# Kernel tuning notes

Measured on AMD Instinct MI355X. Metric: run time of the kernel, lower is better.

## Reference

```python
import jax, jax.numpy as jnp
import numpy as np

B, S, E, H, SN, LMAX = 128, 512, 768, 16, 100, 5
DH = E // H  # 48

def setup_inputs() -> dict:
    key = jax.random.key(0)
    ks = jax.random.split(key, 10)
    idx = jax.random.randint(ks[0], (B, LMAX), 0, S)
    lengths = jax.random.randint(ks[1], (B,), 1, LMAX + 1)
    valid = jnp.arange(LMAX)[None, :] < lengths[:, None]
    locations = jnp.where(valid, idx, -1)
    return {
        "last_hidden_state": jax.random.normal(ks[2], (B, S, E), jnp.float32),
        "sense_emb": jax.random.normal(ks[3], (B, SN, E), jnp.float32),
        "locations": locations,
        "in_proj_weight": jax.random.normal(ks[4], (3 * E, E), jnp.float32) * 0.02,
        "in_proj_bias": jax.random.normal(ks[5], (3 * E,), jnp.float32) * 0.02,
        "out_proj_weight": jax.random.normal(ks[6], (E, E), jnp.float32) * 0.02,
        "out_proj_bias": jax.random.normal(ks[7], (E,), jnp.float32) * 0.02,
        "linear_weight": jax.random.normal(ks[8], (SN, E), jnp.float32) * 0.02,
        "linear_bias": jax.random.normal(ks[9], (SN,), jnp.float32) * 0.02,
    }

def reference(last_hidden_state, sense_emb, locations, in_proj_weight, in_proj_bias,
              out_proj_weight, out_proj_bias, linear_weight, linear_bias):
    # Ragged gather + mean over the valid (non -1) token locations per row.
    mask = (locations != -1)                                   # [B, LMAX]
    safe = jnp.where(mask, locations, 0)                       # [B, LMAX]
    gathered = jnp.take_along_axis(last_hidden_state, safe[..., None], axis=1)  # [B,LMAX,E]
    cnt = mask.sum(axis=1, keepdims=True).astype(last_hidden_state.dtype)
    pun = (gathered * mask[..., None]).sum(axis=1) / cnt       # [B, E]

    # qkv: prepend pun-word embedding to the sense embeddings -> [B, SN+1, E]
    qkv = jnp.concatenate([pun[:, None, :], sense_emb], axis=1)

    # nn.MultiheadAttention with batch_first=False: axis0 = seq (L=B), axis1 = batch (N=SN+1).
    proj = qkv @ in_proj_weight.T + in_proj_bias               # [L, N, 3E]
    q, k, v = jnp.split(proj, 3, axis=-1)
    L, N = qkv.shape[0], qkv.shape[1]
    q = q.reshape(L, N, H, DH) * (DH ** -0.5)
    k = k.reshape(L, N, H, DH)
    v = v.reshape(L, N, H, DH)
    scores = jnp.einsum('lnhd,mnhd->nhlm', q, k)               # [N,H,L,L]
    attn = jax.nn.softmax(scores, axis=-1)
    ctx = jnp.einsum('nhlm,mnhd->lnhd', attn, v).reshape(L, N, E)
    attn_out = ctx @ out_proj_weight.T + out_proj_bias         # [L, N, E]

    res = attn_out[:, 0, :]                                    # [B, E] (batch slot 0)
    res = res @ linear_weight.T + linear_bias                  # [B, SN]
    return res
```

## Files before the change

kernel.cpp:

```cpp
#include <hip/hip_runtime.h>

#define SEQ 512
#define EMB 768
#define K3E 2304
#define DHD 48

__global__ __launch_bounds__(256) void k0_pun(
    const float* __restrict__ lhs, const int* __restrict__ loc,
    float* __restrict__ pun)
{
  int id = blockIdx.x * 256 + threadIdx.x;
  int row = id / 192;
  int ch  = id - row * 192;
  int cnt = 0;
  float4 s = make_float4(0.f, 0.f, 0.f, 0.f);
#pragma unroll
  for (int j = 0; j < 5; j++) {
    int v = loc[row * 5 + j];
    if (v >= 0) {
      float4 wv = *(const float4*)&lhs[((size_t)row * SEQ + v) * EMB + ch * 4];
      s.x += wv.x; s.y += wv.y; s.z += wv.z; s.w += wv.w;
      cnt++;
    }
  }
  float inv = 1.0f / (float)cnt;
  *(float4*)&pun[(size_t)row * EMB + ch * 4] =
      make_float4(s.x * inv, s.y * inv, s.z * inv, s.w * inv);
}

__global__ __launch_bounds__(512, 4) void k1_gemm_wcomb(
    const float* __restrict__ pun, const float* __restrict__ Bw,
    const float* __restrict__ bias, float* __restrict__ C,
    const float* __restrict__ wlin, const float* __restrict__ wout,
    float* __restrict__ wcomb)
{
  __shared__ float lds[12288];
  const int t = threadIdx.x;
  const int w = t >> 6, l = t & 63;
  const int h2 = l >> 5;
  const int tx = l & 7;
  const int ty = (l >> 3) & 3;
  const int gm = l & 15, gq = l >> 4;
  const int bl = l & 31, bh = l >> 5;
  const int kbase = w * 96;
  const int AW = w * 1536, BW = AW + 512;

  float4 aF, bF0, bF1;
  float acc[4][4] = {};

#define STAGE_A(b) {                                                         \
    int Ab = AW + (b) * 256;                                                 \
    lds[Ab + (gq*4+0)*16 + gm] = aF.x;                                       \
    lds[Ab + (gq*4+1)*16 + gm] = aF.y;                                       \
    lds[Ab + (gq*4+2)*16 + gm] = aF.z;                                       \
    lds[Ab + (gq*4+3)*16 + gm] = aF.w; }

#define INNER(b) {                                                           \
    int Ab = AW + (b) * 256, Bb = BW + (b) * 512;                            \
    _Pragma("unroll")                                                        \
    for (int kk = 0; kk < 8; kk++) {                                         \
      int row = kk * 2 + h2;                                                 \
      float4 a  = *(float4*)&lds[Ab + row * 16 + ty * 4];                    \
      float4 bb = *(float4*)&lds[Bb + row * 32 + tx * 4];                    \
      acc[0][0] += a.x*bb.x; acc[0][1] += a.x*bb.y;                          \
      acc[0][2] += a.x*bb.z; acc[0][3] += a.x*bb.w;                          \
      acc[1][0] += a.y*bb.x; acc[1][1] += a.y*bb.y;                          \
      acc[1][2] += a.y*bb.z; acc[1][3] += a.y*bb.w;                          \
      acc[2][0] += a.z*bb.x; acc[2][1] += a.z*bb.y;                          \
      acc[2][2] += a.z*bb.z; acc[2][3] += a.z*bb.w;                          \
      acc[3][0] += a.w*bb.x; acc[3][1] += a.w*bb.y;                          \
      acc[3][2] += a.w*bb.z; acc[3][3] += a.w*bb.w;                          \
    } }

#define FOLD_AND_PARTIAL() {                                                 \
    _Pragma("unroll")                                                        \
    for (int i = 0; i < 4; i++) {                                            \
      _Pragma("unroll")                                                      \
      for (int j = 0; j < 4; j++)                                            \
        acc[i][j] += __shfl_xor(acc[i][j], 32);                              \
    }                                                                        \
    if (l < 32) {                                                            \
      _Pragma("unroll")                                                      \
      for (int i = 0; i < 4; i++)                                            \
        *(float4*)&lds[AW + (ty*4 + i) * 32 + tx * 4] =                      \
            make_float4(acc[i][0], acc[i][1], acc[i][2], acc[i][3]);         \
    }                                                                        \
    __syncthreads(); }

  if (blockIdx.x < 576) {
    const int c  = blockIdx.x;
    const int bm = (c / 72) * 16, bn = (c % 72) * 32;
    const float* arow = pun + (size_t)(bm + gm) * EMB;
    const float* brow = Bw + (size_t)(bn + bl) * EMB;

#define G_LOAD(s) {                                                          \
    int k0 = kbase + (s) * 16;                                               \
    aF  = *(const float4*)&arow[k0 + gq * 4];                                \
    bF0 = *(const float4*)&brow[k0 + bh * 8 + 0];                            \
    bF1 = *(const float4*)&brow[k0 + bh * 8 + 4]; }

#define G_WRITE(b) {                                                         \
    STAGE_A(b)                                                               \
    int Bb = BW + (b) * 512;                                                 \
    lds[Bb + (bh*8+0)*32 + bl] = bF0.x; lds[Bb + (bh*8+1)*32 + bl] = bF0.y;  \
    lds[Bb + (bh*8+2)*32 + bl] = bF0.z; lds[Bb + (bh*8+3)*32 + bl] = bF0.w;  \
    lds[Bb + (bh*8+4)*32 + bl] = bF1.x; lds[Bb + (bh*8+5)*32 + bl] = bF1.y;  \
    lds[Bb + (bh*8+6)*32 + bl] = bF1.z; lds[Bb + (bh*8+7)*32 + bl] = bF1.w; }

    G_LOAD(0); G_WRITE(0);
    for (int s = 0; s < 6; s++) {
      int b = s & 1;
      if (s < 5) G_LOAD(s + 1);
      INNER(b);
      if (s < 5) G_WRITE(b ^ 1);
    }
#undef G_LOAD
#undef G_WRITE

    FOLD_AND_PARTIAL();
    int m = t >> 5, n = t & 31;
    float v = lds[0*1536 + t] + lds[1*1536 + t] + lds[2*1536 + t] + lds[3*1536 + t]
            + lds[4*1536 + t] + lds[5*1536 + t] + lds[6*1536 + t] + lds[7*1536 + t]
            + bias[bn + n];
    C[(size_t)(bm + m) * K3E + bn + n] = v;
  } else {
    const int cc = blockIdx.x - 576;
    const int bm = (cc / 24) * 16, bn = (cc % 24) * 32;
    const int wi = l >> 2;
    const int j4 = (l & 3) * 8;
    int arow_i = bm + gm; if (arow_i > 99) arow_i = 99;
    const float* arow = wlin + (size_t)arow_i * EMB;

#define W_LOAD(s) {                                                          \
    int k0 = kbase + (s) * 16;                                               \
    aF  = *(const float4*)&arow[k0 + gq * 4];                                \
    const float* wr = wout + (size_t)(k0 + wi) * EMB + bn + j4;              \
    bF0 = *(const float4*)&wr[0];                                            \
    bF1 = *(const float4*)&wr[4]; }

#define W_WRITE(b) {                                                         \
    STAGE_A(b)                                                               \
    int Bb = BW + (b) * 512;                                                 \
    *(float4*)&lds[Bb + wi*32 + j4]     = bF0;                               \
    *(float4*)&lds[Bb + wi*32 + j4 + 4] = bF1; }

    W_LOAD(0); W_WRITE(0);
    for (int s = 0; s < 6; s++) {
      int b = s & 1;
      if (s < 5) W_LOAD(s + 1);
      INNER(b);
      if (s < 5) W_WRITE(b ^ 1);
    }
#undef W_LOAD
#undef W_WRITE

    FOLD_AND_PARTIAL();
    int m = t >> 5, n = t & 31;
    if (bm + m < 100) {
      float v = lds[0*1536 + t] + lds[1*1536 + t] + lds[2*1536 + t] + lds[3*1536 + t]
              + lds[4*1536 + t] + lds[5*1536 + t] + lds[6*1536 + t] + lds[7*1536 + t];
      wcomb[(size_t)(bm + m) * EMB + bn + n] = v;
    }
  }
#undef STAGE_A
#undef INNER
#undef FOLD_AND_PARTIAL
}

__global__ __launch_bounds__(256) void k2_attn(
    const float* __restrict__ proj, float* __restrict__ ctx)
{
  __shared__ float ks[128][52];
  __shared__ float vs[128][52];
  int h  = blockIdx.x >> 3;
  int l0 = (blockIdx.x & 7) * 16;
  int t  = threadIdx.x;

  for (int i = t; i < 128 * 12; i += 256) {
    int m  = i / 12;
    int dd = (i - m * 12) * 4;
    float4 kv = *(const float4*)&proj[(size_t)m * K3E + EMB     + h * DHD + dd];
    float4 vv = *(const float4*)&proj[(size_t)m * K3E + 2 * EMB + h * DHD + dd];
    *(float4*)&ks[m][dd] = kv;
    *(float4*)&vs[m][dd] = vv;
  }

  int l  = t >> 4;
  int g  = t & 15;
  int lg = l0 + l;
  const float scale = 0.14433756729740643f;
  float q[48];
#pragma unroll
  for (int jj = 0; jj < 12; jj++) {
    float4 qv = *(const float4*)&proj[(size_t)lg * K3E + h * DHD + jj * 4];
    q[jj*4+0] = qv.x * scale; q[jj*4+1] = qv.y * scale;
    q[jj*4+2] = qv.z * scale; q[jj*4+3] = qv.w * scale;
  }
  __syncthreads();

  float sv[8];
  float smax = -1e30f;
#pragma unroll
  for (int jm = 0; jm < 8; jm++) {
    int m = g + jm * 16;
    float s = 0.0f;
#pragma unroll
    for (int dq = 0; dq < 12; dq++) {
      float4 kv = *(const float4*)&ks[m][dq * 4];
      s += q[dq*4+0]*kv.x + q[dq*4+1]*kv.y + q[dq*4+2]*kv.z + q[dq*4+3]*kv.w;
    }
    sv[jm] = s;
    smax = fmaxf(smax, s);
  }
#pragma unroll
  for (int off = 1; off < 16; off <<= 1) smax = fmaxf(smax, __shfl_xor(smax, off));
  float ssum = 0.0f;
#pragma unroll
  for (int jm = 0; jm < 8; jm++) { float e = __expf(sv[jm] - smax); sv[jm] = e; ssum += e; }
#pragma unroll
  for (int off = 1; off < 16; off <<= 1) ssum += __shfl_xor(ssum, off);
  float inv = 1.0f / ssum;
#pragma unroll
  for (int jm = 0; jm < 8; jm++) sv[jm] *= inv;

  float acc[48] = {};
#pragma unroll
  for (int jm = 0; jm < 8; jm++) {
    int m = g + jm * 16;
    float p = sv[jm];
#pragma unroll
    for (int dq = 0; dq < 12; dq++) {
      float4 vv = *(const float4*)&vs[m][dq * 4];
      acc[dq*4+0] += p*vv.x; acc[dq*4+1] += p*vv.y;
      acc[dq*4+2] += p*vv.z; acc[dq*4+3] += p*vv.w;
    }
  }

  {
    float buf[24];
    if (g & 8) {
#pragma unroll
      for (int d = 0; d < 24; d++) buf[d] = acc[d];
    } else {
#pragma unroll
      for (int d = 0; d < 24; d++) buf[d] = acc[d + 24];
    }
#pragma unroll
    for (int d = 0; d < 24; d++) buf[d] = __shfl_xor(buf[d], 8);
    if (g & 8) {
#pragma unroll
      for (int d = 0; d < 24; d++) acc[d] = acc[d + 24] + buf[d];
    } else {
#pragma unroll
      for (int d = 0; d < 24; d++) acc[d] = acc[d] + buf[d];
    }
  }
  {
    float buf[12];
    if (g & 4) {
#pragma unroll
      for (int d = 0; d < 12; d++) buf[d] = acc[d];
    } else {
#pragma unroll
      for (int d = 0; d < 12; d++) buf[d] = acc[d + 12];
    }
#pragma unroll
    for (int d = 0; d < 12; d++) buf[d] = __shfl_xor(buf[d], 4);
    if (g & 4) {
#pragma unroll
      for (int d = 0; d < 12; d++) acc[d] = acc[d + 12] + buf[d];
    } else {
#pragma unroll
      for (int d = 0; d < 12; d++) acc[d] = acc[d] + buf[d];
    }
  }
  {
    float buf[6];
    if (g & 2) {
#pragma unroll
      for (int d = 0; d < 6; d++) buf[d] = acc[d];
    } else {
#pragma unroll
      for (int d = 0; d < 6; d++) buf[d] = acc[d + 6];
    }
#pragma unroll
    for (int d = 0; d < 6; d++) buf[d] = __shfl_xor(buf[d], 2);
    if (g & 2) {
#pragma unroll
      for (int d = 0; d < 6; d++) acc[d] = acc[d + 6] + buf[d];
    } else {
#pragma unroll
      for (int d = 0; d < 6; d++) acc[d] = acc[d] + buf[d];
    }
  }
  {
    float buf[3];
    if (g & 1) {
#pragma unroll
      for (int d = 0; d < 3; d++) buf[d] = acc[d];
    } else {
#pragma unroll
      for (int d = 0; d < 3; d++) buf[d] = acc[d + 3];
    }
#pragma unroll
    for (int d = 0; d < 3; d++) buf[d] = __shfl_xor(buf[d], 1);
    if (g & 1) {
#pragma unroll
      for (int d = 0; d < 3; d++) acc[d] = acc[d + 3] + buf[d];
    } else {
#pragma unroll
      for (int d = 0; d < 3; d++) acc[d] = acc[d] + buf[d];
    }
  }
#pragma unroll
  for (int j = 0; j < 3; j++) {
    ctx[(size_t)lg * EMB + h * DHD + g * 3 + j] = acc[j];
  }
}

__global__ __launch_bounds__(512, 4) void k3_final(
    const float* __restrict__ A, const float* __restrict__ Bw,
    const float* __restrict__ wlin, const float* __restrict__ bout,
    const float* __restrict__ blin, float* __restrict__ C)
{
  __shared__ float lds[14368];
  const int t = threadIdx.x;
  const int w = t >> 6, l = t & 63;
  const int bm = blockIdx.y * 16, bn = blockIdx.x * 32;
  const int tx = l & 7, ty = l >> 3;
  const int gm = l & 15, gq = l >> 4;
  const int bl = l & 31, bh = l >> 5;
  const int kbase = w * 96;
  const int AW = w * 1792, BW = AW + 640;

  if (t < 256) {
    int col = bn + (t >> 3);
    int ks  = (t & 7) * 96;
    float p = 0.f;
    if (col < 100) {
      const float* wr = wlin + (size_t)col * EMB + ks;
#pragma unroll
      for (int j = 0; j < 24; j++) {
        float4 wv = *(const float4*)&wr[j * 4];
        float4 bv = *(const float4*)&bout[ks + j * 4];
        p += wv.x*bv.x + wv.y*bv.y + wv.z*bv.z + wv.w*bv.w;
      }
    }
    p += __shfl_xor(p, 1); p += __shfl_xor(p, 2); p += __shfl_xor(p, 4);
    if ((t & 7) == 0) lds[14336 + (t >> 3)] = p + (col < 100 ? blin[col] : 0.f);
  }

  const float* arow = A + (size_t)(bm + gm) * EMB;
  int brow_i = bn + bl; if (brow_i > 99) brow_i = 99;
  const float* brow = Bw + (size_t)brow_i * EMB;

  float4 aF, bF0, bF1;

#define F_LOAD(s) {                                                          \
    int k0 = kbase + (s) * 16;                                               \
    aF  = *(const float4*)&arow[k0 + gq * 4];                                \
    bF0 = *(const float4*)&brow[k0 + bh * 8 + 0];                            \
    bF1 = *(const float4*)&brow[k0 + bh * 8 + 4]; }

#define F_WRITE(b) {                                                         \
    int Ab = AW + (b) * 320;                                                 \
    lds[Ab + (gq*4+0)*20 + gm] = aF.x;                                       \
    lds[Ab + (gq*4+1)*20 + gm] = aF.y;                                       \
    lds[Ab + (gq*4+2)*20 + gm] = aF.z;                                       \
    lds[Ab + (gq*4+3)*20 + gm] = aF.w;                                       \
    int Bb = BW + (b) * 576;                                                 \
    lds[Bb + (bh*8+0)*36 + bl] = bF0.x; lds[Bb + (bh*8+1)*36 + bl] = bF0.y;  \
    lds[Bb + (bh*8+2)*36 + bl] = bF0.z; lds[Bb + (bh*8+3)*36 + bl] = bF0.w;  \
    lds[Bb + (bh*8+4)*36 + bl] = bF1.x; lds[Bb + (bh*8+5)*36 + bl] = bF1.y;  \
    lds[Bb + (bh*8+6)*36 + bl] = bF1.z; lds[Bb + (bh*8+7)*36 + bl] = bF1.w; }

  float acc[2][4] = {};
  F_LOAD(0); F_WRITE(0);
  for (int s = 0; s < 6; s++) {
    int b = s & 1;
    if (s < 5) F_LOAD(s + 1);
    int Ab = AW + b * 320, Bb = BW + b * 576;
#pragma unroll
    for (int kk = 0; kk < 16; kk++) {
      float2 a  = *(float2*)&lds[Ab + kk * 20 + ty * 2];
      float4 bb = *(float4*)&lds[Bb + kk * 36 + tx * 4];
      acc[0][0] += a.x*bb.x; acc[0][1] += a.x*bb.y; acc[0][2] += a.x*bb.z; acc[0][3] += a.x*bb.w;
      acc[1][0] += a.y*bb.x; acc[1][1] += a.y*bb.y; acc[1][2] += a.y*bb.z; acc[1][3] += a.y*bb.w;
    }
    if (s < 5) F_WRITE(b ^ 1);
  }
#undef F_LOAD
#undef F_WRITE

#pragma unroll
  for (int i = 0; i < 2; i++)
    *(float4*)&lds[AW + (ty*2 + i) * 32 + tx * 4] =
        make_float4(acc[i][0], acc[i][1], acc[i][2], acc[i][3]);
  __syncthreads();
  int m = t >> 5, n = t & 31;
  int col = bn + n;
  if (col < 100) {
    float v = lds[0*1792 + t] + lds[1*1792 + t] + lds[2*1792 + t] + lds[3*1792 + t]
            + lds[4*1792 + t] + lds[5*1792 + t] + lds[6*1792 + t] + lds[7*1792 + t]
            + lds[14336 + n];
    C[(size_t)(bm + m) * 100 + col] = v;
  }
}

extern "C" void kernel_launch(void* const* d_in, const int* in_sizes, int n_in,
                              void* d_out, int out_size, void* d_ws, size_t ws_size,
                              hipStream_t stream) {
  const float* lhs   = (const float*)d_in[0];
  const int*   loc   = (const int*)  d_in[2];
  const float* w_in  = (const float*)d_in[3];
  const float* b_in  = (const float*)d_in[4];
  const float* w_out = (const float*)d_in[5];
  const float* b_out = (const float*)d_in[6];
  const float* w_lin = (const float*)d_in[7];
  const float* b_lin = (const float*)d_in[8];
  float* out = (float*)d_out;

  char* ws = (char*)d_ws;
  float* pun   = (float*)(ws);
  float* proj  = (float*)(ws + 393216);
  float* ctx   = (float*)(ws + 1572864);
  float* wcomb = (float*)(ws + 1966080);

  k0_pun<<<96, 256, 0, stream>>>(lhs, loc, pun);
  k1_gemm_wcomb<<<744, 512, 0, stream>>>(pun, w_in, b_in, proj,
                                         w_lin, w_out, wcomb);
  k2_attn<<<128, 256, 0, stream>>>(proj, ctx);
  k3_final<<<dim3(4, 8), 512, 0, stream>>>(ctx, wcomb, w_lin, b_out, b_lin, out);
}
```

Measured before the change: 45.58 us.

## Fuse attention and final GEMM into one kernel with per-row-block flag sync

Merges the attention kernel and the final projection GEMM into a single launch of 160 blocks. The first 128 blocks compute attention and bump a per-row-tile counter after writing ctx. The remaining 32 blocks precompute the bias term, spin on that counter, then run the GEMM with 256 threads instead of 512. This removes one kernel launch boundary and lets the final GEMM for a row tile start as soon as its 16 attention blocks finish. The risks are spin-wait deadlock if the consumer blocks occupy slots before the producers run, and the cost of a half-size thread block in the GEMM. Flags are reset in the first kernel.

```diff
diff --git a/kernel.cpp b/kernel.cpp
--- a/kernel.cpp
+++ b/kernel.cpp
@@ -7,8 +7,11 @@
 
 __global__ __launch_bounds__(256) void k0_pun(
     const float* __restrict__ lhs, const int* __restrict__ loc,
-    float* __restrict__ pun)
+    float* __restrict__ pun, int* __restrict__ flags)
 {
+  if (blockIdx.x == 0 && threadIdx.x < 8)
+    __hip_atomic_store(&flags[threadIdx.x], 0, __ATOMIC_RELAXED,
+                       __HIP_MEMORY_SCOPE_AGENT);
   int id = blockIdx.x * 256 + threadIdx.x;
   int row = id / 192;
   int ch  = id - row * 192;
@@ -167,243 +170,261 @@
 #undef FOLD_AND_PARTIAL
 }
 
-__global__ __launch_bounds__(256) void k2_attn(
-    const float* __restrict__ proj, float* __restrict__ ctx)
+__global__ __launch_bounds__(256) void k23_attn_final(
+    const float* __restrict__ proj, const float* __restrict__ wcomb,
+    const float* __restrict__ wlin, const float* __restrict__ bout,
+    const float* __restrict__ blin, float* __restrict__ ctx,
+    float* __restrict__ out, int* __restrict__ flags)
 {
-  __shared__ float ks[128][52];
-  __shared__ float vs[128][52];
-  int h  = blockIdx.x >> 3;
-  int l0 = (blockIdx.x & 7) * 16;
-  int t  = threadIdx.x;
-
-  for (int i = t; i < 128 * 12; i += 256) {
-    int m  = i / 12;
-    int dd = (i - m * 12) * 4;
-    float4 kv = *(const float4*)&proj[(size_t)m * K3E + EMB     + h * DHD + dd];
-    float4 vv = *(const float4*)&proj[(size_t)m * K3E + 2 * EMB + h * DHD + dd];
-    *(float4*)&ks[m][dd] = kv;
-    *(float4*)&vs[m][dd] = vv;
-  }
-
-  int l  = t >> 4;
-  int g  = t & 15;
-  int lg = l0 + l;
-  const float scale = 0.14433756729740643f;
-  float q[48];
-#pragma unroll
-  for (int jj = 0; jj < 12; jj++) {
-    float4 qv = *(const float4*)&proj[(size_t)lg * K3E + h * DHD + jj * 4];
-    q[jj*4+0] = qv.x * scale; q[jj*4+1] = qv.y * scale;
-    q[jj*4+2] = qv.z * scale; q[jj*4+3] = qv.w * scale;
-  }
-  __syncthreads();
-
-  float sv[8];
-  float smax = -1e30f;
-#pragma unroll
-  for (int jm = 0; jm < 8; jm++) {
-    int m = g + jm * 16;
-    float s = 0.0f;
-#pragma unroll
-    for (int dq = 0; dq < 12; dq++) {
-      float4 kv = *(const float4*)&ks[m][dq * 4];
-      s += q[dq*4+0]*kv.x + q[dq*4+1]*kv.y + q[dq*4+2]*kv.z + q[dq*4+3]*kv.w;
-    }
-    sv[jm] = s;
-    smax = fmaxf(smax, s);
-  }
-#pragma unroll
-  for (int off = 1; off < 16; off <<= 1) smax = fmaxf(smax, __shfl_xor(smax, off));
-  float ssum = 0.0f;
-#pragma unroll
-  for (int jm = 0; jm < 8; jm++) { float e = __expf(sv[jm] - smax); sv[jm] = e; ssum += e; }
-#pragma unroll
-  for (int off = 1; off < 16; off <<= 1) ssum += __shfl_xor(ssum, off);
-  float inv = 1.0f / ssum;
-#pragma unroll
-  for (int jm = 0; jm < 8; jm++) sv[jm] *= inv;
-
-  float acc[48] = {};
-#pragma unroll
-  for (int jm = 0; jm < 8; jm++) {
-    int m = g + jm * 16;
-    float p = sv[jm];
-#pragma unroll
-    for (int dq = 0; dq < 12; dq++) {
-      float4 vv = *(const float4*)&vs[m][dq * 4];
-      acc[dq*4+0] += p*vv.x; acc[dq*4+1] += p*vv.y;
-      acc[dq*4+2] += p*vv.z; acc[dq*4+3] += p*vv.w;
-    }
-  }
-
-  {
-    float buf[24];
-    if (g & 8) {
-#pragma unroll
-      for (int d = 0; d < 24; d++) buf[d] = acc[d];
-    } else {
-#pragma unroll
-      for (int d = 0; d < 24; d++) buf[d] = acc[d + 24];
-    }
-#pragma unroll
-    for (int d = 0; d < 24; d++) buf[d] = __shfl_xor(buf[d], 8);
-    if (g & 8) {
-#pragma unroll
-      for (int d = 0; d < 24; d++) acc[d] = acc[d + 24] + buf[d];
-    } else {
-#pragma unroll
-      for (int d = 0; d < 24; d++) acc[d] = acc[d] + buf[d];
-    }
-  }
-  {
-    float buf[12];
-    if (g & 4) {
-#pragma unroll
-      for (int d = 0; d < 12; d++) buf[d] = acc[d];
-    } else {
-#pragma unroll
-      for (int d = 0; d < 12; d++) buf[d] = acc[d + 12];
-    }
-#pragma unroll
-    for (int d = 0; d < 12; d++) buf[d] = __shfl_xor(buf[d], 4);
-    if (g & 4) {
-#pragma unroll
-      for (int d = 0; d < 12; d++) acc[d] = acc[d + 12] + buf[d];
-    } else {
-#pragma unroll
-      for (int d = 0; d < 12; d++) acc[d] = acc[d] + buf[d];
-    }
-  }
-  {
-    float buf[6];
-    if (g & 2) {
-#pragma unroll
-      for (int d = 0; d < 6; d++) buf[d] = acc[d];
-    } else {
-#pragma unroll
-      for (int d = 0; d < 6; d++) buf[d] = acc[d + 6];
-    }
-#pragma unroll
-    for (int d = 0; d < 6; d++) buf[d] = __shfl_xor(buf[d], 2);
-    if (g & 2) {
-#pragma unroll
-      for (int d = 0; d < 6; d++) acc[d] = acc[d + 6] + buf[d];
-    } else {
-#pragma unroll
-      for (int d = 0; d < 6; d++) acc[d] = acc[d] + buf[d];
-    }
-  }
-  {
-    float buf[3];
-    if (g & 1) {
-#pragma unroll
-      for (int d = 0; d < 3; d++) buf[d] = acc[d];
-    } else {
-#pragma unroll
-      for (int d = 0; d < 3; d++) buf[d] = acc[d + 3];
-    }
-#pragma unroll
-    for (int d = 0; d < 3; d++) buf[d] = __shfl_xor(buf[d], 1);
-    if (g & 1) {
-#pragma unroll
-      for (int d = 0; d < 3; d++) acc[d] = acc[d + 3] + buf[d];
-    } else {
-#pragma unroll
-      for (int d = 0; d < 3; d++) acc[d] = acc[d] + buf[d];
-    }
-  }
-#pragma unroll
-  for (int j = 0; j < 3; j++) {
-    ctx[(size_t)lg * EMB + h * DHD + g * 3 + j] = acc[j];
-  }
-}
-
-__global__ __launch_bounds__(512, 4) void k3_final(
-    const float* __restrict__ A, const float* __restrict__ Bw,
-    const float* __restrict__ wlin, const float* __restrict__ bout,
-    const float* __restrict__ blin, float* __restrict__ C)
-{
-  __shared__ float lds[14368];
+  __shared__ float lds[13312];
   const int t = threadIdx.x;
-  const int w = t >> 6, l = t & 63;
-  const int bm = blockIdx.y * 16, bn = blockIdx.x * 32;
-  const int tx = l & 7, ty = l >> 3;
-  const int gm = l & 15, gq = l >> 4;
-  const int bl = l & 31, bh = l >> 5;
-  const int kbase = w * 96;
-  const int AW = w * 1792, BW = AW + 640;
-
-  if (t < 256) {
-    int col = bn + (t >> 3);
-    int ks  = (t & 7) * 96;
-    float p = 0.f;
-    if (col < 100) {
-      const float* wr = wlin + (size_t)col * EMB + ks;
-#pragma unroll
-      for (int j = 0; j < 24; j++) {
-        float4 wv = *(const float4*)&wr[j * 4];
-        float4 bv = *(const float4*)&bout[ks + j * 4];
-        p += wv.x*bv.x + wv.y*bv.y + wv.z*bv.z + wv.w*bv.w;
-      }
-    }
-    p += __shfl_xor(p, 1); p += __shfl_xor(p, 2); p += __shfl_xor(p, 4);
-    if ((t & 7) == 0) lds[14336 + (t >> 3)] = p + (col < 100 ? blin[col] : 0.f);
-  }
-
-  const float* arow = A + (size_t)(bm + gm) * EMB;
-  int brow_i = bn + bl; if (brow_i > 99) brow_i = 99;
-  const float* brow = Bw + (size_t)brow_i * EMB;
-
-  float4 aF, bF0, bF1;
+
+  if (blockIdx.x < 128) {
+    float* ks = lds;
+    float* vs = lds + 6656;
+    int h  = blockIdx.x >> 3;
+    int l0 = (blockIdx.x & 7) * 16;
+
+    for (int i = t; i < 128 * 12; i += 256) {
+      int m  = i / 12;
+      int dd = (i - m * 12) * 4;
+      float4 kv = *(const float4*)&proj[(size_t)m * K3E + EMB     + h * DHD + dd];
+      float4 vv = *(const float4*)&proj[(size_t)m * K3E + 2 * EMB + h * DHD + dd];
+      *(float4*)&ks[m * 52 + dd] = kv;
+      *(float4*)&vs[m * 52 + dd] = vv;
+    }
+
+    int l  = t >> 4;
+    int g  = t & 15;
+    int lg = l0 + l;
+    const float scale = 0.14433756729740643f;
+    float q[48];
+#pragma unroll
+    for (int jj = 0; jj < 12; jj++) {
+      float4 qv = *(const float4*)&proj[(size_t)lg * K3E + h * DHD + jj * 4];
+      q[jj*4+0] = qv.x * scale; q[jj*4+1] = qv.y * scale;
+      q[jj*4+2] = qv.z * scale; q[jj*4+3] = qv.w * scale;
+    }
+    __syncthreads();
+
+    float sv[8];
+    float smax = -1e30f;
+#pragma unroll
+    for (int jm = 0; jm < 8; jm++) {
+      int m = g + jm * 16;
+      float s = 0.0f;
+#pragma unroll
+      for (int dq = 0; dq < 12; dq++) {
+        float4 kv = *(const float4*)&ks[m * 52 + dq * 4];
+        s += q[dq*4+0]*kv.x + q[dq*4+1]*kv.y + q[dq*4+2]*kv.z + q[dq*4+3]*kv.w;
+      }
+      sv[jm] = s;
+      smax = fmaxf(smax, s);
+    }
+#pragma unroll
+    for (int off = 1; off < 16; off <<= 1) smax = fmaxf(smax, __shfl_xor(smax, off));
+    float ssum = 0.0f;
+#pragma unroll
+    for (int jm = 0; jm < 8; jm++) { float e = __expf(sv[jm] - smax); sv[jm] = e; ssum += e; }
+#pragma unroll
+    for (int off = 1; off < 16; off <<= 1) ssum += __shfl_xor(ssum, off);
+    float inv = 1.0f / ssum;
+#pragma unroll
+    for (int jm = 0; jm < 8; jm++) sv[jm] *= inv;
+
+    float acc[48] = {};
+#pragma unroll
+    for (int jm = 0; jm < 8; jm++) {
+      int m = g + jm * 16;
+      float p = sv[jm];
+#pragma unroll
+      for (int dq = 0; dq < 12; dq++) {
+        float4 vv = *(const float4*)&vs[m * 52 + dq * 4];
+        acc[dq*4+0] += p*vv.x; acc[dq*4+1] += p*vv.y;
+        acc[dq*4+2] += p*vv.z; acc[dq*4+3] += p*vv.w;
+      }
+    }
+
+    {
+      float buf[24];
+      if (g & 8) {
+#pragma unroll
+        for (int d = 0; d < 24; d++) buf[d] = acc[d];
+      } else {
+#pragma unroll
+        for (int d = 0; d < 24; d++) buf[d] = acc[d + 24];
+      }
+#pragma unroll
+      for (int d = 0; d < 24; d++) buf[d] = __shfl_xor(buf[d], 8);
+      if (g & 8) {
+#pragma unroll
+        for (int d = 0; d < 24; d++) acc[d] = acc[d + 24] + buf[d];
+      } else {
+#pragma unroll
+        for (int d = 0; d < 24; d++) acc[d] = acc[d] + buf[d];
+      }
+    }
+    {
+      float buf[12];
+      if (g & 4) {
+#pragma unroll
+        for (int d = 0; d < 12; d++) buf[d] = acc[d];
+      } else {
+#pragma unroll
+        for (int d = 0; d < 12; d++) buf[d] = acc[d + 12];
+      }
+#pragma unroll
+      for (int d = 0; d < 12; d++) buf[d] = __shfl_xor(buf[d], 4);
+      if (g & 4) {
+#pragma unroll
+        for (int d = 0; d < 12; d++) acc[d] = acc[d + 12] + buf[d];
+      } else {
+#pragma unroll
+        for (int d = 0; d < 12; d++) acc[d] = acc[d] + buf[d];
+      }
+    }
+    {
+      float buf[6];
+      if (g & 2) {
+#pragma unroll
+        for (int d = 0; d < 6; d++) buf[d] = acc[d];
+      } else {
+#pragma unroll
+        for (int d = 0; d < 6; d++) buf[d] = acc[d + 6];
+      }
+#pragma unroll
+      for (int d = 0; d < 6; d++) buf[d] = __shfl_xor(buf[d], 2);
+      if (g & 2) {
+#pragma unroll
+        for (int d = 0; d < 6; d++) acc[d] = acc[d + 6] + buf[d];
+      } else {
+#pragma unroll
+        for (int d = 0; d < 6; d++) acc[d] = acc[d] + buf[d];
+      }
+    }
+    {
+      float buf[3];
+      if (g & 1) {
+#pragma unroll
+        for (int d = 0; d < 3; d++) buf[d] = acc[d];
+      } else {
+#pragma unroll
+        for (int d = 0; d < 3; d++) buf[d] = acc[d + 3];
+      }
+#pragma unroll
+      for (int d = 0; d < 3; d++) buf[d] = __shfl_xor(buf[d], 1);
+      if (g & 1) {
+#pragma unroll
+        for (int d = 0; d < 3; d++) acc[d] = acc[d + 3] + buf[d];
+      } else {
+#pragma unroll
+        for (int d = 0; d < 3; d++) acc[d] = acc[d] + buf[d];
+      }
+    }
+#pragma unroll
+    for (int j = 0; j < 3; j++) {
+      ctx[(size_t)lg * EMB + h * DHD + g * 3 + j] = acc[j];
+    }
+
+    __syncthreads();
+    if (t == 0) {
+      __threadfence();
+      __hip_atomic_fetch_add(&flags[blockIdx.x & 7], 1, __ATOMIC_RELAXED,
+                             __HIP_MEMORY_SCOPE_AGENT);
+    }
+  } else {
+    const int c  = blockIdx.x - 128;
+    const int bm = (c >> 2) * 16, bn = (c & 3) * 32;
+    const int w  = t >> 6, l = t & 63;
+    const int tx = l & 7, ty = l >> 3;
+    const int am = l & 15, aq = l >> 4;
+    const int bl = l & 31, bh = l >> 5;
+    const int kbase = w * 192;
+    const int AW = w * 1792, BW = AW + 640;
+
+    {
+      int col = bn + (t >> 3);
+      int ks  = (t & 7) * 96;
+      float p = 0.f;
+      if (col < 100) {
+        const float* wr = wlin + (size_t)col * EMB + ks;
+#pragma unroll
+        for (int j = 0; j < 24; j++) {
+          float4 wv = *(const float4*)&wr[j * 4];
+          float4 bv = *(const float4*)&bout[ks + j * 4];
+          p += wv.x*bv.x + wv.y*bv.y + wv.z*bv.z + wv.w*bv.w;
+        }
+      }
+      p += __shfl_xor(p, 1); p += __shfl_xor(p, 2); p += __shfl_xor(p, 4);
+      if ((t & 7) == 0) lds[7168 + (t >> 3)] = p + (col < 100 ? blin[col] : 0.f);
+    }
+
+    if (t == 0) {
+      while (__hip_atomic_load(&flags[bm >> 4], __ATOMIC_RELAXED,
+                               __HIP_MEMORY_SCOPE_AGENT) < 16)
+        __builtin_amdgcn_s_sleep(2);
+      __threadfence();
+    }
+    __syncthreads();
+
+    const float* arow = ctx + (size_t)(bm + am) * EMB;
+    int brow_i = bn + bl; if (brow_i > 99) brow_i = 99;
+    const float* brow = wcomb + (size_t)brow_i * EMB;
+
+    float4 aF, bF0, bF1;
 
 #define F_LOAD(s) {                                                          \
     int k0 = kbase + (s) * 16;                                               \
-    aF  = *(const float4*)&arow[k0 + gq * 4];                                \
+    aF  = *(const float4*)&arow[k0 + aq * 4];                                \
     bF0 = *(const float4*)&brow[k0 + bh * 8 + 0];                            \
     bF1 = *(const float4*)&brow[k0 + bh * 8 + 4]; }
 
 #define F_WRITE(b) {                                                         \
     int Ab = AW + (b) * 320;                                                 \
-    lds[Ab + (gq*4+0)*20 + gm] = aF.x;                                       \
-    lds[Ab + (gq*4+1)*20 + gm] = aF.y;                                       \
-    lds[Ab + (gq*4+2)*20 + gm] = aF.z;                                       \
-    lds[Ab + (gq*4+3)*20 + gm] = aF.w;                                       \
+    lds[Ab + (aq*4+0)*20 + am] = aF.x;                                       \
+    lds[Ab + (aq*4+1)*20 + am] = aF.y;                                       \
+    lds[Ab + (aq*4+2)*20 + am] = aF.z;                                       \
+    lds[Ab + (aq*4+3)*20 + am] = aF.w;                                       \
     int Bb = BW + (b) * 576;                                                 \
     lds[Bb + (bh*8+0)*36 + bl] = bF0.x; lds[Bb + (bh*8+1)*36 + bl] = bF0.y;  \
     lds[Bb + (bh*8+2)*36 + bl] = bF0.z; lds[Bb + (bh*8+3)*36 + bl] = bF0.w;  \
     lds[Bb + (bh*8+4)*36 + bl] = bF1.x; lds[Bb + (bh*8+5)*36 + bl] = bF1.y;  \
     lds[Bb + (bh*8+6)*36 + bl] = bF1.z; lds[Bb + (bh*8+7)*36 + bl] = bF1.w; }
 
-  float acc[2][4] = {};
-  F_LOAD(0); F_WRITE(0);
-  for (int s = 0; s < 6; s++) {
-    int b = s & 1;
-    if (s < 5) F_LOAD(s + 1);
-    int Ab = AW + b * 320, Bb = BW + b * 576;
-#pragma unroll
-    for (int kk = 0; kk < 16; kk++) {
-      float2 a  = *(float2*)&lds[Ab + kk * 20 + ty * 2];
-      float4 bb = *(float4*)&lds[Bb + kk * 36 + tx * 4];
-      acc[0][0] += a.x*bb.x; acc[0][1] += a.x*bb.y; acc[0][2] += a.x*bb.z; acc[0][3] += a.x*bb.w;
-      acc[1][0] += a.y*bb.x; acc[1][1] += a.y*bb.y; acc[1][2] += a.y*bb.z; acc[1][3] += a.y*bb.w;
-    }
-    if (s < 5) F_WRITE(b ^ 1);
-  }
+    float acc[2][4] = {};
+    F_LOAD(0); F_WRITE(0);
+    for (int s = 0; s < 12; s++) {
+      int b = s & 1;
+      if (s < 11) F_LOAD(s + 1);
+      int Ab = AW + b * 320, Bb = BW + b * 576;
+#pragma unroll
+      for (int kk = 0; kk < 16; kk++) {
+        float2 a  = *(float2*)&lds[Ab + kk * 20 + ty * 2];
+        float4 bb = *(float4*)&lds[Bb + kk * 36 + tx * 4];
+        acc[0][0] += a.x*bb.x; acc[0][1] += a.x*bb.y; acc[0][2] += a.x*bb.z; acc[0][3] += a.x*bb.w;
+        acc[1][0] += a.y*bb.x; acc[1][1] += a.y*bb.y; acc[1][2] += a.y*bb.z; acc[1][3] += a.y*bb.w;
+      }
+      if (s < 11) F_WRITE(b ^ 1);
+    }
 #undef F_LOAD
 #undef F_WRITE
 
 #pragma unroll
-  for (int i = 0; i < 2; i++)
-    *(float4*)&lds[AW + (ty*2 + i) * 32 + tx * 4] =
-        make_float4(acc[i][0], acc[i][1], acc[i][2], acc[i][3]);
-  __syncthreads();
-  int m = t >> 5, n = t & 31;
-  int col = bn + n;
-  if (col < 100) {
-    float v = lds[0*1792 + t] + lds[1*1792 + t] + lds[2*1792 + t] + lds[3*1792 + t]
-            + lds[4*1792 + t] + lds[5*1792 + t] + lds[6*1792 + t] + lds[7*1792 + t]
-            + lds[14336 + n];
-    C[(size_t)(bm + m) * 100 + col] = v;
+    for (int i = 0; i < 2; i++)
+      *(float4*)&lds[AW + (ty*2 + i) * 32 + tx * 4] =
+          make_float4(acc[i][0], acc[i][1], acc[i][2], acc[i][3]);
+    __syncthreads();
+    int o = t * 2;
+    int m = o >> 5, n = o & 31;
+#pragma unroll
+    for (int j = 0; j < 2; j++) {
+      int col = bn + n + j;
+      if (col < 100) {
+        float v = lds[0*1792 + o + j] + lds[1*1792 + o + j] +
+                  lds[2*1792 + o + j] + lds[3*1792 + o + j] + lds[7168 + n + j];
+        out[(size_t)(bm + m) * 100 + col] = v;
+      }
+    }
   }
 }
 
@@ -425,10 +446,11 @@
   float* proj  = (float*)(ws + 393216);
   float* ctx   = (float*)(ws + 1572864);
   float* wcomb = (float*)(ws + 1966080);
-
-  k0_pun<<<96, 256, 0, stream>>>(lhs, loc, pun);
+  int*   flags = (int*)  (ws + 2273280);
+
+  k0_pun<<<96, 256, 0, stream>>>(lhs, loc, pun, flags);
   k1_gemm_wcomb<<<744, 512, 0, stream>>>(pun, w_in, b_in, proj,
                                          w_lin, w_out, wcomb);
-  k2_attn<<<128, 256, 0, stream>>>(proj, ctx);
-  k3_final<<<dim3(4, 8), 512, 0, stream>>>(ctx, wcomb, w_lin, b_out, b_lin, out);
+  k23_attn_final<<<160, 256, 0, stream>>>(proj, wcomb, w_lin, b_out, b_lin,
+                                          ctx, out, flags);
 }
```

Measured after the change: 47.85 us. +5.0%, slower.

## Move wcomb weight-product GEMM from QKV projection kernel into attention kernel

Applied to the files above, without the earlier changes.

The wcomb precompute (linear_weight times out_proj_weight), which does not depend on the attention output, moves out of the QKV-projection launch and into the attention launch as 168 extra blocks beside the 128 attention blocks. Its GEMM is retiled for 256 threads: 4 waves each take a 192-wide K slice, padded LDS strides are used, and the reduction writes float2. The aim is to balance work across launches, so the small 128-block attention kernel no longer leaves the GPU mostly idle. The cost is that the merged kernel's shared-memory footprint and register use are set by its larger branch, which may lower occupancy.

```diff
diff --git a/kernel.cpp b/kernel.cpp
--- a/kernel.cpp
+++ b/kernel.cpp
@@ -28,11 +28,9 @@
       make_float4(s.x * inv, s.y * inv, s.z * inv, s.w * inv);
 }
 
-__global__ __launch_bounds__(512, 4) void k1_gemm_wcomb(
+__global__ __launch_bounds__(512, 4) void k1_gemm(
     const float* __restrict__ pun, const float* __restrict__ Bw,
-    const float* __restrict__ bias, float* __restrict__ C,
-    const float* __restrict__ wlin, const float* __restrict__ wout,
-    float* __restrict__ wcomb)
+    const float* __restrict__ bias, float* __restrict__ C)
 {
   __shared__ float lds[12288];
   const int t = threadIdx.x;
@@ -48,12 +46,28 @@
   float4 aF, bF0, bF1;
   float acc[4][4] = {};
 
-#define STAGE_A(b) {                                                         \
+  const int c  = blockIdx.x;
+  const int bm = (c / 72) * 16, bn = (c % 72) * 32;
+  const float* arow = pun + (size_t)(bm + gm) * EMB;
+  const float* brow = Bw + (size_t)(bn + bl) * EMB;
+
+#define G_LOAD(s) {                                                          \
+    int k0 = kbase + (s) * 16;                                               \
+    aF  = *(const float4*)&arow[k0 + gq * 4];                                \
+    bF0 = *(const float4*)&brow[k0 + bh * 8 + 0];                            \
+    bF1 = *(const float4*)&brow[k0 + bh * 8 + 4]; }
+
+#define G_WRITE(b) {                                                         \
     int Ab = AW + (b) * 256;                                                 \
     lds[Ab + (gq*4+0)*16 + gm] = aF.x;                                       \
     lds[Ab + (gq*4+1)*16 + gm] = aF.y;                                       \
     lds[Ab + (gq*4+2)*16 + gm] = aF.z;                                       \
-    lds[Ab + (gq*4+3)*16 + gm] = aF.w; }
+    lds[Ab + (gq*4+3)*16 + gm] = aF.w;                                       \
+    int Bb = BW + (b) * 512;                                                 \
+    lds[Bb + (bh*8+0)*32 + bl] = bF0.x; lds[Bb + (bh*8+1)*32 + bl] = bF0.y;  \
+    lds[Bb + (bh*8+2)*32 + bl] = bF0.z; lds[Bb + (bh*8+3)*32 + bl] = bF0.w;  \
+    lds[Bb + (bh*8+4)*32 + bl] = bF1.x; lds[Bb + (bh*8+5)*32 + bl] = bF1.y;  \
+    lds[Bb + (bh*8+6)*32 + bl] = bF1.z; lds[Bb + (bh*8+7)*32 + bl] = bF1.w; }
 
 #define INNER(b) {                                                           \
     int Ab = AW + (b) * 256, Bb = BW + (b) * 512;                            \
@@ -72,249 +86,257 @@
       acc[3][2] += a.w*bb.z; acc[3][3] += a.w*bb.w;                          \
     } }
 
-#define FOLD_AND_PARTIAL() {                                                 \
-    _Pragma("unroll")                                                        \
-    for (int i = 0; i < 4; i++) {                                            \
-      _Pragma("unroll")                                                      \
-      for (int j = 0; j < 4; j++)                                            \
-        acc[i][j] += __shfl_xor(acc[i][j], 32);                              \
-    }                                                                        \
-    if (l < 32) {                                                            \
-      _Pragma("unroll")                                                      \
-      for (int i = 0; i < 4; i++)                                            \
-        *(float4*)&lds[AW + (ty*4 + i) * 32 + tx * 4] =                      \
-            make_float4(acc[i][0], acc[i][1], acc[i][2], acc[i][3]);         \
-    }                                                                        \
-    __syncthreads(); }
-
-  if (blockIdx.x < 576) {
-    const int c  = blockIdx.x;
-    const int bm = (c / 72) * 16, bn = (c % 72) * 32;
-    const float* arow = pun + (size_t)(bm + gm) * EMB;
-    const float* brow = Bw + (size_t)(bn + bl) * EMB;
-
-#define G_LOAD(s) {                                                          \
-    int k0 = kbase + (s) * 16;                                               \
-    aF  = *(const float4*)&arow[k0 + gq * 4];                                \
-    bF0 = *(const float4*)&brow[k0 + bh * 8 + 0];                            \
-    bF1 = *(const float4*)&brow[k0 + bh * 8 + 4]; }
-
-#define G_WRITE(b) {                                                         \
-    STAGE_A(b)                                                               \
-    int Bb = BW + (b) * 512;                                                 \
-    lds[Bb + (bh*8+0)*32 + bl] = bF0.x; lds[Bb + (bh*8+1)*32 + bl] = bF0.y;  \
-    lds[Bb + (bh*8+2)*32 + bl] = bF0.z; lds[Bb + (bh*8+3)*32 + bl] = bF0.w;  \
-    lds[Bb + (bh*8+4)*32 + bl] = bF1.x; lds[Bb + (bh*8+5)*32 + bl] = bF1.y;  \
-    lds[Bb + (bh*8+6)*32 + bl] = bF1.z; lds[Bb + (bh*8+7)*32 + bl] = bF1.w; }
-
-    G_LOAD(0); G_WRITE(0);
-    for (int s = 0; s < 6; s++) {
-      int b = s & 1;
-      if (s < 5) G_LOAD(s + 1);
-      INNER(b);
-      if (s < 5) G_WRITE(b ^ 1);
-    }
+  G_LOAD(0); G_WRITE(0);
+  for (int s = 0; s < 6; s++) {
+    int b = s & 1;
+    if (s < 5) G_LOAD(s + 1);
+    INNER(b);
+    if (s < 5) G_WRITE(b ^ 1);
+  }
 #undef G_LOAD
 #undef G_WRITE
-
-    FOLD_AND_PARTIAL();
-    int m = t >> 5, n = t & 31;
-    float v = lds[0*1536 + t] + lds[1*1536 + t] + lds[2*1536 + t] + lds[3*1536 + t]
-            + lds[4*1536 + t] + lds[5*1536 + t] + lds[6*1536 + t] + lds[7*1536 + t]
-            + bias[bn + n];
-    C[(size_t)(bm + m) * K3E + bn + n] = v;
+#undef INNER
+
+#pragma unroll
+  for (int i = 0; i < 4; i++) {
+#pragma unroll
+    for (int j = 0; j < 4; j++)
+      acc[i][j] += __shfl_xor(acc[i][j], 32);
+  }
+  if (l < 32) {
+#pragma unroll
+    for (int i = 0; i < 4; i++)
+      *(float4*)&lds[AW + (ty*4 + i) * 32 + tx * 4] =
+          make_float4(acc[i][0], acc[i][1], acc[i][2], acc[i][3]);
+  }
+  __syncthreads();
+  int m = t >> 5, n = t & 31;
+  float v = lds[0*1536 + t] + lds[1*1536 + t] + lds[2*1536 + t] + lds[3*1536 + t]
+          + lds[4*1536 + t] + lds[5*1536 + t] + lds[6*1536 + t] + lds[7*1536 + t]
+          + bias[bn + n];
+  C[(size_t)(bm + m) * K3E + bn + n] = v;
+}
+
+__global__ __launch_bounds__(256) void k2_attn_wcomb(
+    const float* __restrict__ proj, float* __restrict__ ctx,
+    const float* __restrict__ wlin, const float* __restrict__ wout,
+    float* __restrict__ wcomb)
+{
+  __shared__ float lds[13312];
+  const int t = threadIdx.x;
+
+  if (blockIdx.x < 128) {
+    float* ks = lds;
+    float* vs = lds + 6656;
+    int h  = blockIdx.x >> 3;
+    int l0 = (blockIdx.x & 7) * 16;
+
+    for (int i = t; i < 128 * 12; i += 256) {
+      int m  = i / 12;
+      int dd = (i - m * 12) * 4;
+      float4 kv = *(const float4*)&proj[(size_t)m * K3E + EMB     + h * DHD + dd];
+      float4 vv = *(const float4*)&proj[(size_t)m * K3E + 2 * EMB + h * DHD + dd];
+      *(float4*)&ks[m * 52 + dd] = kv;
+      *(float4*)&vs[m * 52 + dd] = vv;
+    }
+
+    int l  = t >> 4;
+    int g  = t & 15;
+    int lg = l0 + l;
+    const float scale = 0.14433756729740643f;
+    float q[48];
+#pragma unroll
+    for (int jj = 0; jj < 12; jj++) {
+      float4 qv = *(const float4*)&proj[(size_t)lg * K3E + h * DHD + jj * 4];
+      q[jj*4+0] = qv.x * scale; q[jj*4+1] = qv.y * scale;
+      q[jj*4+2] = qv.z * scale; q[jj*4+3] = qv.w * scale;
+    }
+    __syncthreads();
+
+    float sv[8];
+    float smax = -1e30f;
+#pragma unroll
+    for (int jm = 0; jm < 8; jm++) {
+      int m = g + jm * 16;
+      float s = 0.0f;
+#pragma unroll
+      for (int dq = 0; dq < 12; dq++) {
+        float4 kv = *(const float4*)&ks[m * 52 + dq * 4];
+        s += q[dq*4+0]*kv.x + q[dq*4+1]*kv.y + q[dq*4+2]*kv.z + q[dq*4+3]*kv.w;
+      }
+      sv[jm] = s;
+      smax = fmaxf(smax, s);
+    }
+#pragma unroll
+    for (int off = 1; off < 16; off <<= 1) smax = fmaxf(smax, __shfl_xor(smax, off));
+    float ssum = 0.0f;
+#pragma unroll
+    for (int jm = 0; jm < 8; jm++) { float e = __expf(sv[jm] - smax); sv[jm] = e; ssum += e; }
+#pragma unroll
+    for (int off = 1; off < 16; off <<= 1) ssum += __shfl_xor(ssum, off);
+    float inv = 1.0f / ssum;
+#pragma unroll
+    for (int jm = 0; jm < 8; jm++) sv[jm] *= inv;
+
+    float acc[48] = {};
+#pragma unroll
+    for (int jm = 0; jm < 8; jm++) {
+      int m = g + jm * 16;
+      float p = sv[jm];
+#pragma unroll
+      for (int dq = 0; dq < 12; dq++) {
+        float4 vv = *(const float4*)&vs[m * 52 + dq * 4];
+        acc[dq*4+0] += p*vv.x; acc[dq*4+1] += p*vv.y;
+        acc[dq*4+2] += p*vv.z; acc[dq*4+3] += p*vv.w;
+      }
+    }
+
+    {
+      float buf[24];
+      if (g & 8) {
+#pragma unroll
+        for (int d = 0; d < 24; d++) buf[d] = acc[d];
+      } else {
+#pragma unroll
+        for (int d = 0; d < 24; d++) buf[d] = acc[d + 24];
+      }
+#pragma unroll
+      for (int d = 0; d < 24; d++) buf[d] = __shfl_xor(buf[d], 8);
+      if (g & 8) {
+#pragma unroll
+        for (int d = 0; d < 24; d++) acc[d] = acc[d + 24] + buf[d];
+      } else {
+#pragma unroll
+        for (int d = 0; d < 24; d++) acc[d] = acc[d] + buf[d];
+      }
+    }
+    {
+      float buf[12];
+      if (g & 4) {
+#pragma unroll
+        for (int d = 0; d < 12; d++) buf[d] = acc[d];
+      } else {
+#pragma unroll
+        for (int d = 0; d < 12; d++) buf[d] = acc[d + 12];
+      }
+#pragma unroll
+      for (int d = 0; d < 12; d++) buf[d] = __shfl_xor(buf[d], 4);
+      if (g & 4) {
+#pragma unroll
+        for (int d = 0; d < 12; d++) acc[d] = acc[d + 12] + buf[d];
+      } else {
+#pragma unroll
+        for (int d = 0; d < 12; d++) acc[d] = acc[d] + buf[d];
+      }
+    }
+    {
+      float buf[6];
+      if (g & 2) {
+#pragma unroll
+        for (int d = 0; d < 6; d++) buf[d] = acc[d];
+      } else {
+#pragma unroll
+        for (int d = 0; d < 6; d++) buf[d] = acc[d + 6];
+      }
+#pragma unroll
+      for (int d = 0; d < 6; d++) buf[d] = __shfl_xor(buf[d], 2);
+      if (g & 2) {
+#pragma unroll
+        for (int d = 0; d < 6; d++) acc[d] = acc[d + 6] + buf[d];
+      } else {
+#pragma unroll
+        for (int d = 0; d < 6; d++) acc[d] = acc[d] + buf[d];
+      }
+    }
+    {
+      float buf[3];
+      if (g & 1) {
+#pragma unroll
+        for (int d = 0; d < 3; d++) buf[d] = acc[d];
+      } else {
+#pragma unroll
+        for (int d = 0; d < 3; d++) buf[d] = acc[d + 3];
+      }
+#pragma unroll
+      for (int d = 0; d < 3; d++) buf[d] = __shfl_xor(buf[d], 1);
+      if (g & 1) {
+#pragma unroll
+        for (int d = 0; d < 3; d++) acc[d] = acc[d + 3] + buf[d];
+      } else {
+#pragma unroll
+        for (int d = 0; d < 3; d++) acc[d] = acc[d] + buf[d];
+      }
+    }
+#pragma unroll
+    for (int j = 0; j < 3; j++) {
+      ctx[(size_t)lg * EMB + h * DHD + g * 3 + j] = acc[j];
+    }
   } else {
-    const int cc = blockIdx.x - 576;
-    const int bm = (cc / 24) * 16, bn = (cc % 24) * 32;
+    const int c  = blockIdx.x - 128;
+    const int bm = (c / 24) * 16, bn = (c % 24) * 32;
+    const int w  = t >> 6, l = t & 63;
+    const int tx = l & 7, ty = l >> 3;
+    const int am = l & 15, aq = l >> 4;
     const int wi = l >> 2;
     const int j4 = (l & 3) * 8;
-    int arow_i = bm + gm; if (arow_i > 99) arow_i = 99;
+    const int kbase = w * 192;
+    const int AW = w * 1792, BW = AW + 640;
+
+    int arow_i = bm + am; if (arow_i > 99) arow_i = 99;
     const float* arow = wlin + (size_t)arow_i * EMB;
+
+    float4 aF, bF0, bF1;
 
 #define W_LOAD(s) {                                                          \
     int k0 = kbase + (s) * 16;                                               \
-    aF  = *(const float4*)&arow[k0 + gq * 4];                                \
+    aF  = *(const float4*)&arow[k0 + aq * 4];                                \
     const float* wr = wout + (size_t)(k0 + wi) * EMB + bn + j4;              \
     bF0 = *(const float4*)&wr[0];                                            \
     bF1 = *(const float4*)&wr[4]; }
 
 #define W_WRITE(b) {                                                         \
-    STAGE_A(b)                                                               \
-    int Bb = BW + (b) * 512;                                                 \
-    *(float4*)&lds[Bb + wi*32 + j4]     = bF0;                               \
-    *(float4*)&lds[Bb + wi*32 + j4 + 4] = bF1; }
-
+    int Ab = AW + (b) * 320;                                                 \
+    lds[Ab + (aq*4+0)*20 + am] = aF.x;                                       \
+    lds[Ab + (aq*4+1)*20 + am] = aF.y;                                       \
+    lds[Ab + (aq*4+2)*20 + am] = aF.z;                                       \
+    lds[Ab + (aq*4+3)*20 + am] = aF.w;                                       \
+    int Bb = BW + (b) * 576;                                                 \
+    *(float4*)&lds[Bb + wi*36 + j4]     = bF0;                               \
+    *(float4*)&lds[Bb + wi*36 + j4 + 4] = bF1; }
+
+    float acc[2][4] = {};
     W_LOAD(0); W_WRITE(0);
-    for (int s = 0; s < 6; s++) {
+    for (int s = 0; s < 12; s++) {
       int b = s & 1;
-      if (s < 5) W_LOAD(s + 1);
-      INNER(b);
-      if (s < 5) W_WRITE(b ^ 1);
+      if (s < 11) W_LOAD(s + 1);
+      int Ab = AW + b * 320, Bb = BW + b * 576;
+#pragma unroll
+      for (int kk = 0; kk < 16; kk++) {
+        float2 a  = *(float2*)&lds[Ab + kk * 20 + ty * 2];
+        float4 bb = *(float4*)&lds[Bb + kk * 36 + tx * 4];
+        acc[0][0] += a.x*bb.x; acc[0][1] += a.x*bb.y; acc[0][2] += a.x*bb.z; acc[0][3] += a.x*bb.w;
+        acc[1][0] += a.y*bb.x; acc[1][1] += a.y*bb.y; acc[1][2] += a.y*bb.z; acc[1][3] += a.y*bb.w;
+      }
+      if (s < 11) W_WRITE(b ^ 1);
     }
 #undef W_LOAD
 #undef W_WRITE
 
-    FOLD_AND_PARTIAL();
-    int m = t >> 5, n = t & 31;
+#pragma unroll
+    for (int i = 0; i < 2; i++)
+      *(float4*)&lds[AW + (ty*2 + i) * 32 + tx * 4] =
+          make_float4(acc[i][0], acc[i][1], acc[i][2], acc[i][3]);
+    __syncthreads();
+    int o = t * 2;
+    int m = o >> 5, n = o & 31;
     if (bm + m < 100) {
-      float v = lds[0*1536 + t] + lds[1*1536 + t] + lds[2*1536 + t] + lds[3*1536 + t]
-              + lds[4*1536 + t] + lds[5*1536 + t] + lds[6*1536 + t] + lds[7*1536 + t];
-      wcomb[(size_t)(bm + m) * EMB + bn + n] = v;
-    }
-  }
-#undef STAGE_A
-#undef INNER
-#undef FOLD_AND_PARTIAL
-}
-
-__global__ __launch_bounds__(256) void k2_attn(
-    const float* __restrict__ proj, float* __restrict__ ctx)
-{
-  __shared__ float ks[128][52];
-  __shared__ float vs[128][52];
-  int h  = blockIdx.x >> 3;
-  int l0 = (blockIdx.x & 7) * 16;
-  int t  = threadIdx.x;
-
-  for (int i = t; i < 128 * 12; i += 256) {
-    int m  = i / 12;
-    int dd = (i - m * 12) * 4;
-    float4 kv = *(const float4*)&proj[(size_t)m * K3E + EMB     + h * DHD + dd];
-    float4 vv = *(const float4*)&proj[(size_t)m * K3E + 2 * EMB + h * DHD + dd];
-    *(float4*)&ks[m][dd] = kv;
-    *(float4*)&vs[m][dd] = vv;
-  }
-
-  int l  = t >> 4;
-  int g  = t & 15;
-  int lg = l0 + l;
-  const float scale = 0.14433756729740643f;
-  float q[48];
-#pragma unroll
-  for (int jj = 0; jj < 12; jj++) {
-    float4 qv = *(const float4*)&proj[(size_t)lg * K3E + h * DHD + jj * 4];
-    q[jj*4+0] = qv.x * scale; q[jj*4+1] = qv.y * scale;
-    q[jj*4+2] = qv.z * scale; q[jj*4+3] = qv.w * scale;
-  }
-  __syncthreads();
-
-  float sv[8];
-  float smax = -1e30f;
-#pragma unroll
-  for (int jm = 0; jm < 8; jm++) {
-    int m = g + jm * 16;
-    float s = 0.0f;
-#pragma unroll
-    for (int dq = 0; dq < 12; dq++) {
-      float4 kv = *(const float4*)&ks[m][dq * 4];
-      s += q[dq*4+0]*kv.x + q[dq*4+1]*kv.y + q[dq*4+2]*kv.z + q[dq*4+3]*kv.w;
-    }
-    sv[jm] = s;
-    smax = fmaxf(smax, s);
-  }
-#pragma unroll
-  for (int off = 1; off < 16; off <<= 1) smax = fmaxf(smax, __shfl_xor(smax, off));
-  float ssum = 0.0f;
-#pragma unroll
-  for (int jm = 0; jm < 8; jm++) { float e = __expf(sv[jm] - smax); sv[jm] = e; ssum += e; }
-#pragma unroll
-  for (int off = 1; off < 16; off <<= 1) ssum += __shfl_xor(ssum, off);
-  float inv = 1.0f / ssum;
-#pragma unroll
-  for (int jm = 0; jm < 8; jm++) sv[jm] *= inv;
-
-  float acc[48] = {};
-#pragma unroll
-  for (int jm = 0; jm < 8; jm++) {
-    int m = g + jm * 16;
-    float p = sv[jm];
-#pragma unroll
-    for (int dq = 0; dq < 12; dq++) {
-      float4 vv = *(const float4*)&vs[m][dq * 4];
-      acc[dq*4+0] += p*vv.x; acc[dq*4+1] += p*vv.y;
-      acc[dq*4+2] += p*vv.z; acc[dq*4+3] += p*vv.w;
-    }
-  }
-
-  {
-    float buf[24];
-    if (g & 8) {
-#pragma unroll
-      for (int d = 0; d < 24; d++) buf[d] = acc[d];
-    } else {
-#pragma unroll
-      for (int d = 0; d < 24; d++) buf[d] = acc[d + 24];
-    }
-#pragma unroll
-    for (int d = 0; d < 24; d++) buf[d] = __shfl_xor(buf[d], 8);
-    if (g & 8) {
-#pragma unroll
-      for (int d = 0; d < 24; d++) acc[d] = acc[d + 24] + buf[d];
-    } else {
-#pragma unroll
-      for (int d = 0; d < 24; d++) acc[d] = acc[d] + buf[d];
-    }
-  }
-  {
-    float buf[12];
-    if (g & 4) {
-#pragma unroll
-      for (int d = 0; d < 12; d++) buf[d] = acc[d];
-    } else {
-#pragma unroll
-      for (int d = 0; d < 12; d++) buf[d] = acc[d + 12];
-    }
-#pragma unroll
-    for (int d = 0; d < 12; d++) buf[d] = __shfl_xor(buf[d], 4);
-    if (g & 4) {
-#pragma unroll
-      for (int d = 0; d < 12; d++) acc[d] = acc[d + 12] + buf[d];
-    } else {
-#pragma unroll
-      for (int d = 0; d < 12; d++) acc[d] = acc[d] + buf[d];
-    }
-  }
-  {
-    float buf[6];
-    if (g & 2) {
-#pragma unroll
-      for (int d = 0; d < 6; d++) buf[d] = acc[d];
-    } else {
-#pragma unroll
-      for (int d = 0; d < 6; d++) buf[d] = acc[d + 6];
-    }
-#pragma unroll
-    for (int d = 0; d < 6; d++) buf[d] = __shfl_xor(buf[d], 2);
-    if (g & 2) {
-#pragma unroll
-      for (int d = 0; d < 6; d++) acc[d] = acc[d + 6] + buf[d];
-    } else {
-#pragma unroll
-      for (int d = 0; d < 6; d++) acc[d] = acc[d] + buf[d];
-    }
-  }
-  {
-    float buf[3];
-    if (g & 1) {
-#pragma unroll
-      for (int d = 0; d < 3; d++) buf[d] = acc[d];
-    } else {
-#pragma unroll
-      for (int d = 0; d < 3; d++) buf[d] = acc[d + 3];
-    }
-#pragma unroll
-    for (int d = 0; d < 3; d++) buf[d] = __shfl_xor(buf[d], 1);
-    if (g & 1) {
-#pragma unroll
-      for (int d = 0; d < 3; d++) acc[d] = acc[d + 3] + buf[d];
-    } else {
-#pragma unroll
-      for (int d = 0; d < 3; d++) acc[d] = acc[d] + buf[d];
-    }
-  }
-#pragma unroll
-  for (int j = 0; j < 3; j++) {
-    ctx[(size_t)lg * EMB + h * DHD + g * 3 + j] = acc[j];
+      float2 s0 = *(float2*)&lds[0*1792 + o];
+      float2 s1 = *(float2*)&lds[1*1792 + o];
+      float2 s2 = *(float2*)&lds[2*1792 + o];
+      float2 s3 = *(float2*)&lds[3*1792 + o];
+      float2 r = make_float2(s0.x+s1.x+s2.x+s3.x, s0.y+s1.y+s2.y+s3.y);
+      *(float2*)&wcomb[(size_t)(bm + m) * EMB + bn + n] = r;
+    }
   }
 }
 
@@ -427,8 +449,7 @@
   float* wcomb = (float*)(ws + 1966080);
 
   k0_pun<<<96, 256, 0, stream>>>(lhs, loc, pun);
-  k1_gemm_wcomb<<<744, 512, 0, stream>>>(pun, w_in, b_in, proj,
-                                         w_lin, w_out, wcomb);
-  k2_attn<<<128, 256, 0, stream>>>(proj, ctx);
+  k1_gemm<<<576, 512, 0, stream>>>(pun, w_in, b_in, proj);
+  k2_attn_wcomb<<<296, 256, 0, stream>>>(proj, ctx, w_lin, w_out, wcomb);
   k3_final<<<dim3(4, 8), 512, 0, stream>>>(ctx, wcomb, w_lin, b_out, b_lin, out);
 }
```

New measurement: 46.49 us. About the same (+2.0%).
